# Performance work log

Measured on AMD Instinct MI355X. Metric: run time of the kernel, lower is better.

The kernel has to match this reference:

```python
import jax, jax.numpy as jnp
import numpy as np

B, S, E, H = 4, 2048, 768, 12
D = E // H  # 64

def setup_inputs() -> dict:
    key = jax.random.key(0)
    k1, k2, k3, k4, k5 = jax.random.split(key, 5)
    x = jax.random.normal(k1, (B, S, E), dtype=jnp.float32)
    att_mask = jnp.ones((B, S), dtype=jnp.int32)
    # parameters (stored transposed vs torch: [in, out])
    W_attn = jax.random.normal(k2, (E, 3 * E), dtype=jnp.float32) * (1.0 / np.sqrt(E))
    b_attn = jax.random.normal(k3, (3 * E,), dtype=jnp.float32) * 0.02
    W_proj = jax.random.normal(k4, (E, E), dtype=jnp.float32) * (1.0 / np.sqrt(E))
    b_proj = jax.random.normal(k5, (E,), dtype=jnp.float32) * 0.02
    return {"x": x, "W_attn": W_attn, "b_attn": b_attn,
            "W_proj": W_proj, "b_proj": b_proj, "att_mask": att_mask}

def reference(x, W_attn, b_attn, W_proj, b_proj, att_mask):
    b, s, e = x.shape
    qkv = x @ W_attn + b_attn                       # [B,S,3E]
    q, k, v = jnp.split(qkv, 3, axis=-1)
    # [B,H,S,D]
    q = q.reshape(b, s, H, D).transpose(0, 2, 1, 3)
    k = k.reshape(b, s, H, D).transpose(0, 2, 1, 3)
    v = v.reshape(b, s, H, D).transpose(0, 2, 1, 3)
    att = jnp.einsum('bhqd,bhkd->bhqk', q, k) * (1.0 / np.sqrt(D))
    causal = jnp.tril(jnp.ones((s, s), dtype=bool))          # [S,S]
    mask = causal[None, None] & (att_mask[:, None, None, :] != 0)  # [B,1,S,S]
    att = jnp.where(mask, att, -jnp.inf)
    att = jax.nn.softmax(att, axis=-1)
    y = jnp.einsum('bhqk,bhkd->bhqd', att, v)       # [B,H,S,D]
    y = y.transpose(0, 2, 1, 3).reshape(b, s, e)
    return y @ W_proj + b_proj
```

## Files before the change

### kernel.cpp

```cpp
#include <hip/hip_runtime.h>
#include <cstdint>


typedef __bf16 bf16x8 __attribute__((ext_vector_type(8)));
typedef __bf16 bf16x4 __attribute__((ext_vector_type(4)));
typedef float  f32x4  __attribute__((ext_vector_type(4)));
typedef float  f32x16 __attribute__((ext_vector_type(16)));

#define MFMA16(a, b, c) __builtin_amdgcn_mfma_f32_16x16x32_bf16(a, b, c, 0, 0, 0)
#define MFMA32(a, b, c) __builtin_amdgcn_mfma_f32_32x32x16_bf16(a, b, c, 0, 0, 0)

static constexpr int Bb = 4, Ss = 2048, Ee = 768, Hh = 12, Dd = 64;
#define QSCALE 0.18033688011112042f

__device__ __forceinline__ void gl2lds16(const void* g, void* l) {
  __builtin_amdgcn_global_load_lds(
      (const __attribute__((address_space(1))) void*)g,
      (__attribute__((address_space(3))) void*)l, 16, 0, 0);
}

__device__ __forceinline__ float fexp2(float x) {
#if __has_builtin(__builtin_amdgcn_exp2f)
  return __builtin_amdgcn_exp2f(x);
#else
  return exp2f(x);
#endif
}

__device__ __forceinline__ int swap23(int x) {
  return (x & ~12) | ((x & 4) << 1) | ((x & 8) >> 1);
}

__global__ void cast_f32_bf16(const float* __restrict__ x,
                              __bf16* __restrict__ y, int n) {
  int i = (blockIdx.x * blockDim.x + threadIdx.x) * 4;
  if (i < n) {
    float4 v = *(const float4*)(x + i);
    bf16x4 o = {(__bf16)v.x, (__bf16)v.y, (__bf16)v.z, (__bf16)v.w};
    *(bf16x4*)(y + i) = o;
  }
}

__global__ void transpose_cast(const float* __restrict__ W,
                               __bf16* __restrict__ Wt, int K, int N) {
  __shared__ float t[64][65];
  const int k0 = blockIdx.y * 64, n0 = blockIdx.x * 64;
#pragma unroll
  for (int i = 0; i < 16; ++i) {
    int lin = i * 256 + threadIdx.x;
    int r = lin >> 6, c = lin & 63;
    t[r][c] = W[(size_t)(k0 + r) * N + n0 + c];
  }
  __syncthreads();
#pragma unroll
  for (int i = 0; i < 16; ++i) {
    int lin = i * 256 + threadIdx.x;
    int r = lin >> 6, c = lin & 63;
    Wt[(size_t)(n0 + r) * K + k0 + c] = (__bf16)t[c][r];
  }
}

template <int MODE>
__global__ __launch_bounds__(256) void gemm_bt(
    const __bf16* __restrict__ A, const __bf16* __restrict__ Bt,
    const float* __restrict__ bias, __bf16* __restrict__ Qb,
    __bf16* __restrict__ Kb, __bf16* __restrict__ VTb,
    float* __restrict__ out, int K, int N) {
  __shared__ __align__(16) __bf16 As[128 * 32];
  __shared__ __align__(16) __bf16 Bs[128 * 32];
  const int tid = threadIdx.x;
  const int wave = tid >> 6, lane = tid & 63;
  const int quad = lane >> 4, c16 = lane & 15;
  const int m0 = blockIdx.y * 128, n0 = blockIdx.x * 128;
  const int wm = (wave >> 1) * 64, wn = (wave & 1) * 64;

  f32x4 acc[4][4] = {};

  for (int k0 = 0; k0 < K; k0 += 32) {
    __syncthreads();
#pragma unroll
    for (int i = 0; i < 2; ++i) {
      const int cb = (i * 4 + wave) * 64;
      const int c = cb + lane;
      const int row = c >> 2, kk = (c & 3) * 8;
      gl2lds16(&A[(size_t)(m0 + row) * K + k0 + kk], &As[cb * 8]);
      gl2lds16(&Bt[(size_t)(n0 + row) * K + k0 + kk], &Bs[cb * 8]);
    }
    __syncthreads();
    bf16x8 af[4], bf[4];
#pragma unroll
    for (int mi = 0; mi < 4; ++mi)
      af[mi] = *(const bf16x8*)&As[(wm + mi * 16 + c16) * 32 + quad * 8];
#pragma unroll
    for (int ni = 0; ni < 4; ++ni)
      bf[ni] = *(const bf16x8*)&Bs[(wn + ni * 16 + c16) * 32 + quad * 8];
#pragma unroll
    for (int mi = 0; mi < 4; ++mi)
#pragma unroll
      for (int ni = 0; ni < 4; ++ni)
        acc[mi][ni] = MFMA16(af[mi], bf[ni], acc[mi][ni]);
  }

#pragma unroll
  for (int mi = 0; mi < 4; ++mi) {
#pragma unroll
    for (int ni = 0; ni < 4; ++ni) {
      const int gcol = n0 + wn + ni * 16 + c16;
      const float bv = bias[gcol];
      const int growb = m0 + wm + mi * 16 + quad * 4;
      if (MODE == 0) {
        const int which = gcol / Ee;
        const int e = gcol - which * Ee;
        const int hh = e >> 6, dd = e & 63;
        const int bb = growb >> 11, ss = growb & 2047;
        const size_t bh = (size_t)(bb * Hh + hh);
        if (which == 2) {
          const int ssp = swap23(ss);
          bf16x4 o;
#pragma unroll
          for (int r = 0; r < 4; ++r) o[r] = (__bf16)(acc[mi][ni][r] + bv);
          *(bf16x4*)&VTb[(bh * Dd + dd) * Ss + ssp] = o;
        } else if (which == 0) {
          const int ddp = swap23(dd);
#pragma unroll
          for (int r = 0; r < 4; ++r)
            Qb[(bh * Ss + ss + r) * Dd + ddp] =
                (__bf16)((acc[mi][ni][r] + bv) * QSCALE);
        } else {
          const int ddp = swap23(dd);
#pragma unroll
          for (int r = 0; r < 4; ++r)
            Kb[(bh * Ss + ss + r) * Dd + ddp] = (__bf16)(acc[mi][ni][r] + bv);
        }
      } else {
#pragma unroll
        for (int r = 0; r < 4; ++r)
          out[(size_t)(growb + r) * N + gcol] = acc[mi][ni][r] + bv;
      }
    }
  }
}

__global__ __launch_bounds__(256, 3) void flash_attn(
    const __bf16* __restrict__ Qb, const __bf16* __restrict__ Kb,
    const __bf16* __restrict__ VTb, const int* __restrict__ amask,
    __bf16* __restrict__ Yb) {
  const int bid = blockIdx.x;
  const int xcd = bid & 7, j = bid >> 3;
  const int bh = xcd * 6 + (j >> 4);
  const int bidx = j & 15;
  const int b = bh / Hh, h = bh - b * Hh;
  const int tid = threadIdx.x, w = tid >> 6, lane = tid & 63;
  const int hl = lane >> 5, l31 = lane & 31;
  const int r7 = l31 & 7;

  const int s = ((w & 2) << 4) + ((w & 1) ? 31 - bidx : bidx);
  const int qs = s * 32;
  const int qg = qs + l31;
  const int ktmax = s >> 1;
  const int nkt = ((63 - bidx) >> 1) + 1;

  const __bf16* Qp = Qb + (size_t)bh * Ss * Dd;
  const __bf16* Kp = Kb + (size_t)bh * Ss * Dd;
  const __bf16* Vp = VTb + (size_t)bh * Dd * Ss;

  __shared__ __align__(16) __bf16 Ksh[3 * 64 * 64];
  __shared__ __align__(16) __bf16 Vsh[3 * 64 * 64];
  __shared__ uint64_t ballots[32];

  bf16x8 qf[4];
#pragma unroll
  for (int wd = 0; wd < 4; ++wd)
    qf[wd] = *(const bf16x8*)&Qp[(size_t)qg * Dd + wd * 16 + hl * 8];

#pragma unroll
  for (int i = 0; i < 8; ++i) {
    const int t = w * 8 + i;
    const uint64_t ball = __ballot(amask[b * Ss + t * 64 + lane] != 0);
    if (lane == 0) ballots[t] = ball;
  }
  asm volatile("s_waitcnt lgkmcnt(0)" ::: "memory");

  auto stage = [&](int kt, int buf) {
    __bf16* kb = &Ksh[buf * 4096];
    __bf16* vb = &Vsh[buf * 4096];
    const char* ksrc = (const char*)(Kp + (size_t)kt * 64 * Dd);
    const char* vsrc = (const char*)Vp + (size_t)kt * 128;
#pragma unroll
    for (int i = 0; i < 2; ++i) {
      const int cb = i * 256 + w * 64;
      const int p = cb + lane;
      const int row = p >> 3;
      const int cc = (p & 7) ^ (row & 7);
      gl2lds16(ksrc + (size_t)row * 128 + cc * 16, &kb[cb * 8]);
      gl2lds16(vsrc + (size_t)row * 4096 + cc * 16, &vb[cb * 8]);
    }
  };

  stage(0, 0);
  if (nkt > 1) stage(1, 1);

  f32x16 yacc[2] = {};
  float m_i = -30000.f, l_i = 0.f;

  for (int kt = 0; kt < nkt; ++kt) {
    if (kt + 1 < nkt)
      asm volatile("s_waitcnt vmcnt(4)\n\ts_barrier" ::: "memory");
    else
      asm volatile("s_waitcnt vmcnt(0)\n\ts_barrier" ::: "memory");
    if (kt + 2 < nkt) stage(kt + 2, (kt + 2) % 3);

    if (kt > ktmax) continue;
    const int k0 = kt * 64;
    const __bf16* kb = &Ksh[(kt % 3) * 4096];
    const __bf16* vb = &Vsh[(kt % 3) * 4096];

    f32x16 sg[2];
#pragma unroll
    for (int g = 0; g < 2; ++g) {
      f32x16 acc = {};
#pragma unroll
      for (int wd = 0; wd < 4; ++wd) {
        const bf16x8 kf = *(const bf16x8*)&kb[(g * 32 + l31) * 64 +
                                             (((2 * wd + hl) ^ r7) * 8)];
        acc = MFMA32(kf, qf[wd], acc);
      }
      sg[g] = acc;
    }

    if (k0 + 63 > qs) {
#pragma unroll
      for (int g = 0; g < 2; ++g)
#pragma unroll
        for (int r = 0; r < 16; ++r) {
          const int key = k0 + g * 32 + (r & 3) + 8 * (r >> 2) + 4 * hl;
          sg[g][r] = (key <= qg) ? sg[g][r] : -30000.f;
        }
    }
    const uint64_t mball = ballots[kt];
    if (mball != ~0ull) {
#pragma unroll
      for (int g = 0; g < 2; ++g)
#pragma unroll
        for (int r = 0; r < 16; ++r) {
          const int kr = g * 32 + (r & 3) + 8 * (r >> 2) + 4 * hl;
          sg[g][r] = ((mball >> kr) & 1) ? sg[g][r] : -30000.f;
        }
    }

    float mx = sg[0][0];
#pragma unroll
    for (int r = 1; r < 16; ++r) mx = fmaxf(mx, sg[0][r]);
#pragma unroll
    for (int r = 0; r < 16; ++r) mx = fmaxf(mx, sg[1][r]);
    mx = fmaxf(mx, __shfl_xor(mx, 32));
    const float mnew = fmaxf(m_i, mx);
    const float alpha = fexp2(m_i - mnew);
    float rs = 0.f;
#pragma unroll
    for (int g = 0; g < 2; ++g)
#pragma unroll
      for (int r = 0; r < 16; ++r) {
        const float e = fexp2(sg[g][r] - mnew);
        sg[g][r] = e;
        rs += e;
      }
    rs += __shfl_xor(rs, 32);
    l_i = l_i * alpha + rs;
    m_i = mnew;
#pragma unroll
    for (int dt = 0; dt < 2; ++dt)
#pragma unroll
      for (int r = 0; r < 16; ++r) yacc[dt][r] *= alpha;

    bf16x8 pf[4];
#pragma unroll
    for (int W = 0; W < 4; ++W) {
      bf16x8 f;
#pragma unroll
      for (int jj = 0; jj < 8; ++jj)
        f[jj] = (__bf16)sg[W >> 1][8 * (W & 1) + jj];
      pf[W] = f;
    }

#pragma unroll
    for (int dt = 0; dt < 2; ++dt)
#pragma unroll
      for (int W = 0; W < 4; ++W) {
        const bf16x8 vf = *(const bf16x8*)&vb[(dt * 32 + l31) * 64 +
                                             (((2 * W + hl) ^ r7) * 8)];
        yacc[dt] = MFMA32(vf, pf[W], yacc[dt]);
      }
  }

  const float inv = 1.f / l_i;
  __bf16* yrow = Yb + (size_t)(b * Ss + qg) * Ee + h * Dd;
#pragma unroll
  for (int dt = 0; dt < 2; ++dt)
#pragma unroll
    for (int sreg = 0; sreg < 4; ++sreg) {
      bf16x4 o;
#pragma unroll
      for (int r = 0; r < 4; ++r)
        o[r] = (__bf16)(yacc[dt][sreg * 4 + r] * inv);
      *(bf16x4*)&yrow[dt * 32 + sreg * 8 + hl * 4] = o;
    }
}

extern "C" void kernel_launch(void* const* d_in, const int* in_sizes, int n_in,
                              void* d_out, int out_size, void* d_ws,
                              size_t ws_size, hipStream_t stream) {
  const float* x      = (const float*)d_in[0];
  const float* W_attn = (const float*)d_in[1];
  const float* b_attn = (const float*)d_in[2];
  const float* W_proj = (const float*)d_in[3];
  const float* b_proj = (const float*)d_in[4];
  const int* att_mask = (const int*)d_in[5];
  float* out = (float*)d_out;

  char* ws = (char*)d_ws;
  __bf16* xb  = (__bf16*)(ws);
  __bf16* Wat = (__bf16*)(ws + 12582912);
  __bf16* Wpt = (__bf16*)(ws + 16121856);
  __bf16* Qb  = (__bf16*)(ws + 17301504);
  __bf16* Kb  = (__bf16*)(ws + 29884416);
  __bf16* VTb = (__bf16*)(ws + 42467328);
  __bf16* Yb  = xb;

  cast_f32_bf16<<<6144, 256, 0, stream>>>(x, xb, Bb * Ss * Ee);
  transpose_cast<<<dim3(36, 12), 256, 0, stream>>>(W_attn, Wat, Ee, 3 * Ee);
  transpose_cast<<<dim3(12, 12), 256, 0, stream>>>(W_proj, Wpt, Ee, Ee);

  gemm_bt<0><<<dim3(18, 64), 256, 0, stream>>>(xb, Wat, b_attn, Qb, Kb, VTb,
                                               nullptr, Ee, 3 * Ee);
  flash_attn<<<768, 256, 0, stream>>>(Qb, Kb, VTb, att_mask, Yb);
  gemm_bt<1><<<dim3(6, 64), 256, 0, stream>>>(Yb, Wpt, b_proj, nullptr,
                                              nullptr, nullptr, out, Ee, Ee);
}
```

Baseline: 230.8 us.

## Drop LDS staging in flash attention, read K/V directly from global memory

Removes the triple-buffered global-to-LDS staging of K and V tiles, along with the shared barriers and precomputed mask ballots. Each wave now loads K and V fragments straight from global memory and builds its mask ballot per tile, iterating only up to its own causal limit with a per-block rotated role assignment. The softmax also gains a lazy rescale: the running max is updated only when a new max exceeds the old one by a threshold, and the max and sum reductions become tree reductions. This removes block-level synchronisation and lets waves run independently, but gives up cross-wave reuse of K/V through LDS, which raises global and cache traffic.

```diff
diff --git a/kernel.cpp b/kernel.cpp
--- a/kernel.cpp
+++ b/kernel.cpp
@@ -152,68 +152,30 @@
   const int b = bh / Hh, h = bh - b * Hh;
   const int tid = threadIdx.x, w = tid >> 6, lane = tid & 63;
   const int hl = lane >> 5, l31 = lane & 31;
-  const int r7 = l31 & 7;
-
-  const int s = ((w & 2) << 4) + ((w & 1) ? 31 - bidx : bidx);
+
+  const int role = (w + bidx) & 3;
+  const int s = ((role & 2) << 4) + ((role & 1) ? 31 - bidx : bidx);
   const int qs = s * 32;
   const int qg = qs + l31;
   const int ktmax = s >> 1;
-  const int nkt = ((63 - bidx) >> 1) + 1;
 
   const __bf16* Qp = Qb + (size_t)bh * Ss * Dd;
   const __bf16* Kp = Kb + (size_t)bh * Ss * Dd;
   const __bf16* Vp = VTb + (size_t)bh * Dd * Ss;
-
-  __shared__ __align__(16) __bf16 Ksh[3 * 64 * 64];
-  __shared__ __align__(16) __bf16 Vsh[3 * 64 * 64];
-  __shared__ uint64_t ballots[32];
+  const int* mp = amask + b * Ss;
 
   bf16x8 qf[4];
 #pragma unroll
   for (int wd = 0; wd < 4; ++wd)
     qf[wd] = *(const bf16x8*)&Qp[(size_t)qg * Dd + wd * 16 + hl * 8];
 
-#pragma unroll
-  for (int i = 0; i < 8; ++i) {
-    const int t = w * 8 + i;
-    const uint64_t ball = __ballot(amask[b * Ss + t * 64 + lane] != 0);
-    if (lane == 0) ballots[t] = ball;
-  }
-  asm volatile("s_waitcnt lgkmcnt(0)" ::: "memory");
-
-  auto stage = [&](int kt, int buf) {
-    __bf16* kb = &Ksh[buf * 4096];
-    __bf16* vb = &Vsh[buf * 4096];
-    const char* ksrc = (const char*)(Kp + (size_t)kt * 64 * Dd);
-    const char* vsrc = (const char*)Vp + (size_t)kt * 128;
-#pragma unroll
-    for (int i = 0; i < 2; ++i) {
-      const int cb = i * 256 + w * 64;
-      const int p = cb + lane;
-      const int row = p >> 3;
-      const int cc = (p & 7) ^ (row & 7);
-      gl2lds16(ksrc + (size_t)row * 128 + cc * 16, &kb[cb * 8]);
-      gl2lds16(vsrc + (size_t)row * 4096 + cc * 16, &vb[cb * 8]);
-    }
-  };
-
-  stage(0, 0);
-  if (nkt > 1) stage(1, 1);
-
   f32x16 yacc[2] = {};
   float m_i = -30000.f, l_i = 0.f;
 
-  for (int kt = 0; kt < nkt; ++kt) {
-    if (kt + 1 < nkt)
-      asm volatile("s_waitcnt vmcnt(4)\n\ts_barrier" ::: "memory");
-    else
-      asm volatile("s_waitcnt vmcnt(0)\n\ts_barrier" ::: "memory");
-    if (kt + 2 < nkt) stage(kt + 2, (kt + 2) % 3);
-
-    if (kt > ktmax) continue;
+  for (int kt = 0; kt <= ktmax; ++kt) {
     const int k0 = kt * 64;
-    const __bf16* kb = &Ksh[(kt % 3) * 4096];
-    const __bf16* vb = &Vsh[(kt % 3) * 4096];
+
+    const uint64_t mball = __ballot(mp[k0 + lane] != 0);
 
     f32x16 sg[2];
 #pragma unroll
@@ -221,8 +183,8 @@
       f32x16 acc = {};
 #pragma unroll
       for (int wd = 0; wd < 4; ++wd) {
-        const bf16x8 kf = *(const bf16x8*)&kb[(g * 32 + l31) * 64 +
-                                             (((2 * wd + hl) ^ r7) * 8)];
+        const bf16x8 kf = *(const bf16x8*)&Kp[(size_t)(k0 + g * 32 + l31) * Dd +
+                                              wd * 16 + hl * 8];
         acc = MFMA32(kf, qf[wd], acc);
       }
       sg[g] = acc;
@@ -237,7 +199,6 @@
           sg[g][r] = (key <= qg) ? sg[g][r] : -30000.f;
         }
     }
-    const uint64_t mball = ballots[kt];
     if (mball != ~0ull) {
 #pragma unroll
       for (int g = 0; g < 2; ++g)
@@ -248,30 +209,45 @@
         }
     }
 
-    float mx = sg[0][0];
-#pragma unroll
-    for (int r = 1; r < 16; ++r) mx = fmaxf(mx, sg[0][r]);
-#pragma unroll
-    for (int r = 0; r < 16; ++r) mx = fmaxf(mx, sg[1][r]);
-    mx = fmaxf(mx, __shfl_xor(mx, 32));
-    const float mnew = fmaxf(m_i, mx);
-    const float alpha = fexp2(m_i - mnew);
-    float rs = 0.f;
-#pragma unroll
-    for (int g = 0; g < 2; ++g)
-#pragma unroll
-      for (int r = 0; r < 16; ++r) {
-        const float e = fexp2(sg[g][r] - mnew);
-        sg[g][r] = e;
-        rs += e;
-      }
-    rs += __shfl_xor(rs, 32);
-    l_i = l_i * alpha + rs;
-    m_i = mnew;
-#pragma unroll
-    for (int dt = 0; dt < 2; ++dt)
-#pragma unroll
-      for (int r = 0; r < 16; ++r) yacc[dt][r] *= alpha;
+    float tm[16];
+#pragma unroll
+    for (int r = 0; r < 16; ++r) tm[r] = fmaxf(sg[0][r], sg[1][r]);
+#pragma unroll
+    for (int off = 8; off >= 1; off >>= 1)
+#pragma unroll
+      for (int r = 0; r < 8; ++r)
+        if (r < off) tm[r] = fmaxf(tm[r], tm[r + off]);
+    const float mx = fmaxf(tm[0], __shfl_xor(tm[0], 32));
+
+    const bool grow = !__all(mx <= m_i + 11.5f);
+    const float mnew = grow ? fmaxf(m_i, mx) : m_i;
+
+    float ts[16];
+#pragma unroll
+    for (int r = 0; r < 16; ++r) {
+      const float e0 = fexp2(sg[0][r] - mnew);
+      const float e1 = fexp2(sg[1][r] - mnew);
+      sg[0][r] = e0;
+      sg[1][r] = e1;
+      ts[r] = e0 + e1;
+    }
+#pragma unroll
+    for (int off = 8; off >= 1; off >>= 1)
+#pragma unroll
+      for (int r = 0; r < 8; ++r)
+        if (r < off) ts[r] += ts[r + off];
+    float rs = ts[0] + __shfl_xor(ts[0], 32);
+
+    if (grow) {
+      const float alpha = fexp2(m_i - mnew);
+      l_i *= alpha;
+      m_i = mnew;
+#pragma unroll
+      for (int dt = 0; dt < 2; ++dt)
+#pragma unroll
+        for (int r = 0; r < 16; ++r) yacc[dt][r] *= alpha;
+    }
+    l_i += rs;
 
     bf16x8 pf[4];
 #pragma unroll
@@ -287,8 +263,8 @@
     for (int dt = 0; dt < 2; ++dt)
 #pragma unroll
       for (int W = 0; W < 4; ++W) {
-        const bf16x8 vf = *(const bf16x8*)&vb[(dt * 32 + l31) * 64 +
-                                             (((2 * W + hl) ^ r7) * 8)];
+        const bf16x8 vf = *(const bf16x8*)&Vp[(size_t)(dt * 32 + l31) * Ss +
+                                              k0 + W * 16 + hl * 8];
         yacc[dt] = MFMA32(vf, pf[W], yacc[dt]);
       }
   }
```

After: 274.3 us. +18.9%, slower.

## Add lazy softmax rescaling, tree reductions, MFMA priority hints, and rotated wave roles

Applied to the files above, without the earlier changes.

The online softmax now skips updating the running max and rescaling the accumulator unless some lane's new max exceeds the old one by more than a threshold, so most key tiles avoid the alpha multiply. The max and sum reductions become tree-shaped to shorten dependency chains. s_setprio raises wave priority around the MFMA blocks so matrix work interleaves with other waves' softmax, and the query-tile-to-wave assignment rotates with the block index to balance causal work across SIMDs. The lazy rescale lets exponentials grow to about 2^11.5 before renormalising, which trades some bf16 precision margin for fewer operations.

```diff
diff --git a/kernel.cpp b/kernel.cpp
--- a/kernel.cpp
+++ b/kernel.cpp
@@ -154,7 +154,8 @@
   const int hl = lane >> 5, l31 = lane & 31;
   const int r7 = l31 & 7;
 
-  const int s = ((w & 2) << 4) + ((w & 1) ? 31 - bidx : bidx);
+  const int role = (w + bidx) & 3;
+  const int s = ((role & 2) << 4) + ((role & 1) ? 31 - bidx : bidx);
   const int qs = s * 32;
   const int qg = qs + l31;
   const int ktmax = s >> 1;
@@ -216,6 +217,7 @@
     const __bf16* vb = &Vsh[(kt % 3) * 4096];
 
     f32x16 sg[2];
+    __builtin_amdgcn_s_setprio(1);
 #pragma unroll
     for (int g = 0; g < 2; ++g) {
       f32x16 acc = {};
@@ -227,6 +229,7 @@
       }
       sg[g] = acc;
     }
+    __builtin_amdgcn_s_setprio(0);
 
     if (k0 + 63 > qs) {
 #pragma unroll
@@ -248,30 +251,45 @@
         }
     }
 
-    float mx = sg[0][0];
-#pragma unroll
-    for (int r = 1; r < 16; ++r) mx = fmaxf(mx, sg[0][r]);
-#pragma unroll
-    for (int r = 0; r < 16; ++r) mx = fmaxf(mx, sg[1][r]);
-    mx = fmaxf(mx, __shfl_xor(mx, 32));
-    const float mnew = fmaxf(m_i, mx);
-    const float alpha = fexp2(m_i - mnew);
-    float rs = 0.f;
-#pragma unroll
-    for (int g = 0; g < 2; ++g)
-#pragma unroll
-      for (int r = 0; r < 16; ++r) {
-        const float e = fexp2(sg[g][r] - mnew);
-        sg[g][r] = e;
-        rs += e;
-      }
-    rs += __shfl_xor(rs, 32);
-    l_i = l_i * alpha + rs;
-    m_i = mnew;
-#pragma unroll
-    for (int dt = 0; dt < 2; ++dt)
-#pragma unroll
-      for (int r = 0; r < 16; ++r) yacc[dt][r] *= alpha;
+    float tm[16];
+#pragma unroll
+    for (int r = 0; r < 16; ++r) tm[r] = fmaxf(sg[0][r], sg[1][r]);
+#pragma unroll
+    for (int off = 8; off >= 1; off >>= 1)
+#pragma unroll
+      for (int r = 0; r < 8; ++r)
+        if (r < off) tm[r] = fmaxf(tm[r], tm[r + off]);
+    const float mx = fmaxf(tm[0], __shfl_xor(tm[0], 32));
+
+    const bool grow = !__all(mx <= m_i + 11.5f);
+    const float mnew = grow ? fmaxf(m_i, mx) : m_i;
+
+    float ts[16];
+#pragma unroll
+    for (int r = 0; r < 16; ++r) {
+      const float e0 = fexp2(sg[0][r] - mnew);
+      const float e1 = fexp2(sg[1][r] - mnew);
+      sg[0][r] = e0;
+      sg[1][r] = e1;
+      ts[r] = e0 + e1;
+    }
+#pragma unroll
+    for (int off = 8; off >= 1; off >>= 1)
+#pragma unroll
+      for (int r = 0; r < 8; ++r)
+        if (r < off) ts[r] += ts[r + off];
+    const float rs = ts[0] + __shfl_xor(ts[0], 32);
+
+    if (grow) {
+      const float alpha = fexp2(m_i - mnew);
+      l_i *= alpha;
+      m_i = mnew;
+#pragma unroll
+      for (int dt = 0; dt < 2; ++dt)
+#pragma unroll
+        for (int r = 0; r < 16; ++r) yacc[dt][r] *= alpha;
+    }
+    l_i += rs;
 
     bf16x8 pf[4];
 #pragma unroll
@@ -283,6 +301,7 @@
       pf[W] = f;
     }
 
+    __builtin_amdgcn_s_setprio(1);
 #pragma unroll
     for (int dt = 0; dt < 2; ++dt)
 #pragma unroll
@@ -291,6 +310,7 @@
                                              (((2 * W + hl) ^ r7) * 8)];
         yacc[dt] = MFMA32(vf, pf[W], yacc[dt]);
       }
+    __builtin_amdgcn_s_setprio(0);
   }
 
   const float inv = 1.f / l_i;
```

Measured after the change: 231.0 us. Within noise of the previous version (+0.1%).
